# Optimization experiments

Hardware: AMD Instinct MI355X
Metric: run time of the kernel (lower is better)

## Reference

```python
import jax, jax.numpy as jnp
import numpy as np

B, N, K, H = 4, 2048, 30, 128
NODE_IN, EDGE_IN, FF = 21, 16, 4 * H


def _normalize(t, axis=-1):
    d = t / jnp.linalg.norm(t, axis=axis, keepdims=True)
    return jnp.where(jnp.isnan(d), 0.0, d)


def gather_nodes(nodes, idx):
    # nodes: [B,N,C], idx: [B,N,K] -> [B,N,K,C]
    b, n, k = idx.shape
    flat = idx.reshape(b, n * k)
    out = jnp.take_along_axis(nodes, flat[:, :, None], axis=1)
    return out.reshape(b, n, k, nodes.shape[-1])


def cal_dihedral(Xf, eps=1e-7):
    dX = Xf[:, 1:, :] - Xf[:, :-1, :]
    U = _normalize(dX)
    u0, u1, u2 = U[:, :-2], U[:, 1:-1], U[:, 2:]
    n0 = _normalize(jnp.cross(u0, u1))
    n1 = _normalize(jnp.cross(u1, u2))
    cosD = jnp.clip((n0 * n1).sum(-1), -1 + eps, 1 - eps)
    v = _normalize(jnp.cross(n0, n1))
    return jnp.sign((-v * u1).sum(-1)) * jnp.arccos(cosD)


def dihedrals(X, eps=1e-7):
    b, n = X.shape[0], X.shape[1]
    Xf = X[:, :, :3, :].reshape(b, 3 * n, 3)
    D = cal_dihedral(Xf)
    D = jnp.pad(D, ((0, 0), (1, 2))).reshape(b, n, 3)
    dihed = jnp.concatenate([jnp.cos(D), jnp.sin(D)], -1)
    dX = Xf[:, 1:] - Xf[:, :-1]
    U = _normalize(dX)
    cosA = jnp.clip((U[:, :-2] * U[:, 1:-1]).sum(-1), -1 + eps, 1 - eps)
    A = jnp.pad(jnp.arccos(cosA), ((0, 0), (1, 2))).reshape(b, n, 3)
    ang = jnp.concatenate([jnp.cos(A), jnp.sin(A)], -1)
    return jnp.concatenate([dihed, ang], -1)  # [B,N,12]


def quaternions(R):
    diag = jnp.diagonal(R, axis1=-2, axis2=-1)
    Rxx, Ryy, Rzz = diag[..., 0], diag[..., 1], diag[..., 2]
    mags = 0.5 * jnp.sqrt(jnp.abs(1 + jnp.stack([Rxx - Ryy - Rzz, -Rxx + Ryy - Rzz, -Rxx - Ryy + Rzz], -1)))
    signs = jnp.sign(jnp.stack([R[..., 2, 1] - R[..., 1, 2], R[..., 0, 2] - R[..., 2, 0], R[..., 1, 0] - R[..., 0, 1]], -1))
    xyz = signs * mags
    w = jnp.sqrt(jax.nn.relu(1 + diag.sum(-1, keepdims=True))) / 2.0
    return _normalize(jnp.concatenate([xyz, w], -1))


def orientations(X, E_idx):
    V = X  # [B,N,4,3]
    b, n = X.shape[0], X.shape[1]
    k = E_idx.shape[2]
    Xf = X[:, :, :3, :].reshape(b, 3 * n, 3)
    dX = Xf[:, 1:] - Xf[:, :-1]
    U = _normalize(dX)
    u0, u1 = U[:, :-2], U[:, 1:-1]
    n0 = _normalize(jnp.cross(u0, u1))[:, ::3]
    b1 = _normalize(u0 - u1)[:, ::3]
    Xa = Xf[:, ::3]  # [B,N,3]
    Q = jnp.stack([b1, n0, jnp.cross(b1, n0)], 2)  # [B,N-1,3,3]
    Q = Q.reshape(b, Q.shape[1], 9)
    Q = jnp.pad(Q, ((0, 0), (0, 1), (0, 0)))  # [B,N,9]
    Qn = gather_nodes(Q, E_idx).reshape(b, n, k, 3, 3)
    Xn = gather_nodes(V[:, :, 1, :], E_idx)
    Nn = gather_nodes(V[:, :, 0, :], E_idx)
    Cn = gather_nodes(V[:, :, 2, :], E_idx)
    On = gather_nodes(V[:, :, 3, :], E_idx)
    Q3 = Q.reshape(b, n, 3, 3)
    dXn = jnp.stack([Xn, Nn, Cn, On], 3) - Xa[:, :, None, None, :]  # [B,N,K,4,3]
    dU = jnp.einsum('bnij,bnkaj->bnkai', Q3, dXn)
    E_direct = _normalize(dU).reshape(b, n, k, 12)
    R = jnp.einsum('bnji,bnkjl->bnkil', Q3, Qn)  # Q^T @ Q_neighbors
    q = quaternions(R)  # [B,N,K,4]
    dX_inner = V[:, :, jnp.array([0, 2, 3]), :] - Xa[:, :, None, :]
    dU_inner = _normalize(jnp.einsum('bnij,bnaj->bnai', Q3, dX_inner))
    V_direct = dU_inner.reshape(b, n, 9)
    return V_direct, E_direct, q


def layernorm(x, g, bta, eps=1e-5):
    m = x.mean(-1, keepdims=True)
    v = ((x - m) ** 2).mean(-1, keepdims=True)
    return (x - m) / jnp.sqrt(v + eps) * g + bta


def gelu(x):
    return jax.nn.gelu(x, approximate=False)


def forward(X, E_idx, Wv_w, Wv_b, We_w, We_b, W1_w, W1_b, W2_w, W2_b, W3_w, W3_b,
            Wi_w, Wi_b, Wo_w, Wo_b, ln1_g, ln1_b, ln2_g, ln2_b):
    k = E_idx.shape[2]
    Dfeat = dihedrals(X)                     # [B,N,12]
    Vd, Ed, q = orientations(X, E_idx)       # [B,N,9],[B,N,K,12],[B,N,K,4]
    hV = jnp.concatenate([Dfeat, Vd], -1) @ Wv_w + Wv_b     # [B,N,H]
    hE = jnp.concatenate([Ed, q], -1) @ We_w + We_b         # [B,N,K,H]
    hV_nbr = gather_nodes(hV, E_idx)                        # [B,N,K,H]
    hV_exp = jnp.broadcast_to(hV[:, :, None, :], hV_nbr.shape)
    hEV = jnp.concatenate([hV_exp, hE, hV_nbr], -1)         # [B,N,K,3H]
    msg = gelu(hEV @ W1_w + W1_b)
    msg = gelu(msg @ W2_w + W2_b)
    msg = msg @ W3_w + W3_b
    dh = msg.sum(-2) / k
    hV = layernorm(hV + dh, ln1_g, ln1_b)
    ff = gelu(hV @ Wi_w + Wi_b) @ Wo_w + Wo_b
    hV = layernorm(hV + ff, ln2_g, ln2_b)
    return hV


def _lin(key, fan_in, fan_out):
    s = 1.0 / np.sqrt(fan_in)
    kw, kb = jax.random.split(key)
    return (jax.random.uniform(kw, (fan_in, fan_out), minval=-s, maxval=s),
            jax.random.uniform(kb, (fan_out,), minval=-s, maxval=s))


def setup_inputs() -> dict:
    key = jax.random.key(0)
    ks = jax.random.split(key, 10)
    X = jax.random.normal(ks[0], (B, N, 4, 3), dtype=jnp.float32) * 3.0
    E_idx = jax.random.randint(ks[1], (B, N, K), 0, N)
    Wv_w, Wv_b = _lin(ks[2], NODE_IN, H)
    We_w, We_b = _lin(ks[3], EDGE_IN, H)
    W1_w, W1_b = _lin(ks[4], 3 * H, H)
    W2_w, W2_b = _lin(ks[5], H, H)
    W3_w, W3_b = _lin(ks[6], H, H)
    Wi_w, Wi_b = _lin(ks[7], H, FF)
    Wo_w, Wo_b = _lin(ks[8], FF, H)
    return {
        'X': X, 'E_idx': E_idx,
        'Wv_w': Wv_w, 'Wv_b': Wv_b, 'We_w': We_w, 'We_b': We_b,
        'W1_w': W1_w, 'W1_b': W1_b, 'W2_w': W2_w, 'W2_b': W2_b,
        'W3_w': W3_w, 'W3_b': W3_b, 'Wi_w': Wi_w, 'Wi_b': Wi_b,
        'Wo_w': Wo_w, 'Wo_b': Wo_b,
        'ln1_g': jnp.ones((H,), jnp.float32), 'ln1_b': jnp.zeros((H,), jnp.float32),
        'ln2_g': jnp.ones((H,), jnp.float32), 'ln2_b': jnp.zeros((H,), jnp.float32),
    }


def reference(X, E_idx, Wv_w, Wv_b, We_w, We_b, W1_w, W1_b, W2_w, W2_b, W3_w, W3_b,
              Wi_w, Wi_b, Wo_w, Wo_b, ln1_g, ln1_b, ln2_g, ln2_b):
    return forward(X, E_idx, Wv_w, Wv_b, We_w, We_b, W1_w, W1_b, W2_w, W2_b,
                   W3_w, W3_b, Wi_w, Wi_b, Wo_w, Wo_b, ln1_g, ln1_b, ln2_g, ln2_b)
```

## Files before the change

kernel.cpp:

```cpp
#include <hip/hip_runtime.h>
#include <math.h>

#define BB 4
#define NN 2048
#define KNB 30
#define HH 128
#define FFD 512

typedef __attribute__((ext_vector_type(4))) float  f32x4;
typedef __attribute__((ext_vector_type(8))) short  s16x8;
typedef __attribute__((ext_vector_type(4))) short  s16x4;

struct F3 { float x,y,z; };
__device__ __forceinline__ F3 f3(float a,float b,float c){ F3 r; r.x=a; r.y=b; r.z=c; return r; }
__device__ __forceinline__ F3 sub3(F3 a, F3 b){ return f3(a.x-b.x, a.y-b.y, a.z-b.z); }
__device__ __forceinline__ float dot3(F3 a, F3 b){ return a.x*b.x + a.y*b.y + a.z*b.z; }
__device__ __forceinline__ F3 cross3(F3 a, F3 b){
  return f3(a.y*b.z-a.z*b.y, a.z*b.x-a.x*b.z, a.x*b.y-a.y*b.x);
}
__device__ __forceinline__ F3 nrm3(F3 a){
  float n2 = dot3(a,a);
  if (n2 <= 0.f) return f3(0.f,0.f,0.f);
  float inv = 1.0f/sqrtf(n2);
  return f3(a.x*inv, a.y*inv, a.z*inv);
}
__device__ __forceinline__ float sgnf(float x){ return (x>0.f)?1.f:((x<0.f)?-1.f:0.f); }
__device__ __forceinline__ float clip1(float x){
  const float e = 1e-7f;
  return fminf(fmaxf(x, -1.f+e), 1.f-e);
}
__device__ __forceinline__ float fgelu(float x){
  float x2 = x*x;
  float t = __builtin_fmaf(-0.1029641763f, x2, -2.302344055f);
  float d = 1.f + __builtin_amdgcn_exp2f(t*x);
  return x * __builtin_amdgcn_rcpf(d);
}
__device__ __forceinline__ short f2bf(float x){
  union { float f; unsigned u; } v; v.f = x;
  unsigned r = v.u + 0x7fffu + ((v.u >> 16) & 1u);
  return (short)(r >> 16);
}

__global__ void k_init(const float* __restrict__ X, float* __restrict__ Qws,
                       float* __restrict__ featws,
                       const float* __restrict__ We, const float* __restrict__ Web,
                       const float* __restrict__ W1, const float* __restrict__ W2,
                       const float* __restrict__ Wi, const float* __restrict__ Wo,
                       const float* __restrict__ W3,
                       short* __restrict__ wfoldT, float* __restrict__ bfold,
                       short* __restrict__ w2t, short* __restrict__ w1aT,
                       short* __restrict__ w1cT, short* __restrict__ wiT,
                       short* __restrict__ woT, short* __restrict__ w3T){
  if (blockIdx.x < 32){
    int t = blockIdx.x*256 + threadIdx.x;
    int b = t / NN, n = t % NN;
    const float* Xb = X + (size_t)b*NN*12;
    #define LD3(r,a) f3(Xb[((r)*4+(a))*3+0], Xb[((r)*4+(a))*3+1], Xb[((r)*4+(a))*3+2])
    F3 x0=LD3(n,0), x1=LD3(n,1), x2=LD3(n,2), x3=LD3(n,3);
    F3 U[5];
    U[1]=nrm3(sub3(x1,x0));
    U[2]=nrm3(sub3(x2,x1));
    if (n>0){ F3 p = LD3(n-1,2); U[0]=nrm3(sub3(x0,p)); } else U[0]=f3(0.f,0.f,0.f);
    if (n<NN-1){ F3 y0=LD3(n+1,0), y1=LD3(n+1,1); U[3]=nrm3(sub3(y0,x2)); U[4]=nrm3(sub3(y1,y0)); }
    else { U[3]=f3(0.f,0.f,0.f); U[4]=f3(0.f,0.f,0.f); }

    float feat[21];
    #pragma unroll
    for (int tt=0; tt<3; tt++){
      bool valid = (n>0 || tt>0) && (n<NN-1 || tt==0);
      if (valid){
        F3 a=U[tt], bv=U[tt+1], c=U[tt+2];
        F3 n0=nrm3(cross3(a,bv)), n1=nrm3(cross3(bv,c));
        float cd = clip1(dot3(n0,n1));
        F3 v = nrm3(cross3(n0,n1));
        float s = sgnf(-dot3(v,bv));
        feat[tt]   = (s==0.f) ? 1.f : cd;
        feat[3+tt] = s*sqrtf(fmaxf(1.f-cd*cd, 0.f));
        float ca = clip1(dot3(a,bv));
        feat[6+tt] = ca;
        feat[9+tt] = sqrtf(fmaxf(1.f-ca*ca, 0.f));
      } else {
        feat[tt]=1.f; feat[3+tt]=0.f; feat[6+tt]=1.f; feat[9+tt]=0.f;
      }
    }
    float Q[9];
    if (n<NN-1){
      F3 b1=nrm3(sub3(U[1],U[2]));
      F3 n0=nrm3(cross3(U[1],U[2]));
      F3 r2=cross3(b1,n0);
      Q[0]=b1.x;Q[1]=b1.y;Q[2]=b1.z;Q[3]=n0.x;Q[4]=n0.y;Q[5]=n0.z;Q[6]=r2.x;Q[7]=r2.y;Q[8]=r2.z;
    } else {
      #pragma unroll
      for (int i=0;i<9;i++) Q[i]=0.f;
    }
    float* qp = Qws + (size_t)t*9;
    #pragma unroll
    for (int i=0;i<9;i++) qp[i]=Q[i];

    feat[12]=0.f; feat[13]=0.f; feat[14]=0.f;
    F3 d1=sub3(x2,x0), d2=sub3(x3,x0);
    F3 r1 = nrm3(f3(Q[0]*d1.x+Q[1]*d1.y+Q[2]*d1.z,
                    Q[3]*d1.x+Q[4]*d1.y+Q[5]*d1.z,
                    Q[6]*d1.x+Q[7]*d1.y+Q[8]*d1.z));
    F3 r2v= nrm3(f3(Q[0]*d2.x+Q[1]*d2.y+Q[2]*d2.z,
                    Q[3]*d2.x+Q[4]*d2.y+Q[5]*d2.z,
                    Q[6]*d2.x+Q[7]*d2.y+Q[8]*d2.z));
    feat[15]=r1.x; feat[16]=r1.y; feat[17]=r1.z;
    feat[18]=r2v.x; feat[19]=r2v.y; feat[20]=r2v.z;
    float* fp = featws + (size_t)t*21;
    #pragma unroll
    for (int i=0;i<21;i++) fp[i]=feat[i];
    #undef LD3
    return;
  }
  int t = (blockIdx.x-32)*256 + threadIdx.x;
  if (t < 2048){
    int c = t >> 4, j = t & 15;
    float a = 0.f;
    for (int k=0;k<HH;k++) a += We[j*HH+k]*W1[(HH+k)*HH + c];
    wfoldT[t] = f2bf(a);
  } else if (t < 2176){
    int c = t - 2048;
    float a = 0.f;
    for (int k=0;k<HH;k++) a += Web[k]*W1[(HH+k)*HH + c];
    bfold[c] = a;
  } else if (t < 18560){
    int i = t - 2176;  int n = i >> 7, k = i & 127;
    w2t[n*HH + k] = f2bf(W2[k*HH + n]);
  } else if (t < 34944){
    int i = t - 18560; int n = i >> 7, k = i & 127;
    w1aT[n*HH + k] = f2bf(W1[k*HH + n]);
  } else if (t < 51328){
    int i = t - 34944; int n = i >> 7, k = i & 127;
    w1cT[n*HH + k] = f2bf(W1[(256+k)*HH + n]);
  } else if (t < 116864){
    int i = t - 51328; int n = i >> 7, k = i & 127;
    wiT[n*HH + k] = f2bf(Wi[k*FFD + n]);
  } else if (t < 182400){
    int i = t - 116864; int k = i >> 7, n = i & 127;
    woT[n*FFD + k] = f2bf(Wo[k*HH + n]);
  } else if (t < 198784){
    int i = t - 182400; int n = i >> 7, k = i & 127;
    w3T[n*HH + k] = f2bf(W3[k*HH + n]);
  }
}

#define ENB 8
#define PNB 32
__global__ void k_ep(const float* __restrict__ X, const int* __restrict__ Eidx,
                     const float* __restrict__ Qws, short* __restrict__ efB,
                     const float* __restrict__ featws, const float* __restrict__ Wv,
                     const float* __restrict__ Wvb, const short* __restrict__ w1aT,
                     const short* __restrict__ w1cT, const float* __restrict__ W1b,
                     const float* __restrict__ bfold, float* __restrict__ hVws,
                     float* __restrict__ Sws, float* __restrict__ Gws){
  const int tid = threadIdx.x;
  if (blockIdx.x < BB*NN/ENB){
    const int nn = tid >> 5, slot = tid & 31;
    const int gnode = blockIdx.x*ENB + nn;
    const int b = gnode >> 11;
    const int n = gnode & (NN-1);
    const int bofs = b*NN;
    short out[16];
    if (slot < KNB){
      int j = Eidx[(size_t)gnode*KNB + slot];
      const float* Qs = Qws + (size_t)gnode*9;
      float q[9];
      #pragma unroll
      for (int i=0;i<9;i++) q[i]=Qs[i];
      const float* Xb = X + (size_t)b*NN*12;
      F3 Xa = f3(Xb[n*12+0], Xb[n*12+1], Xb[n*12+2]);
      const float* Xn = Xb + (size_t)j*12;
      F3 A[4];
      A[0] = f3(Xn[3],  Xn[4],  Xn[5]);
      A[1] = f3(Xn[0],  Xn[1],  Xn[2]);
      A[2] = f3(Xn[6],  Xn[7],  Xn[8]);
      A[3] = f3(Xn[9],  Xn[10], Xn[11]);
      #pragma unroll
      for (int a=0;a<4;a++){
        F3 d = sub3(A[a], Xa);
        F3 w = f3(q[0]*d.x+q[1]*d.y+q[2]*d.z,
                  q[3]*d.x+q[4]*d.y+q[5]*d.z,
                  q[6]*d.x+q[7]*d.y+q[8]*d.z);
        F3 wn = nrm3(w);
        out[a*3+0] = f2bf(wn.x);
        out[a*3+1] = f2bf(wn.y);
        out[a*3+2] = f2bf(wn.z);
      }
      const float* Qn = Qws + (size_t)(bofs + j)*9;
      float p[9];
      #pragma unroll
      for (int i=0;i<9;i++) p[i]=Qn[i];
      float R00=q[0]*p[0]+q[3]*p[3]+q[6]*p[6];
      float R01=q[0]*p[1]+q[3]*p[4]+q[6]*p[7];
      float R02=q[0]*p[2]+q[3]*p[5]+q[6]*p[8];
      float R10=q[1]*p[0]+q[4]*p[3]+q[7]*p[6];
      float R11=q[1]*p[1]+q[4]*p[4]+q[7]*p[7];
      float R12=q[1]*p[2]+q[4]*p[5]+q[7]*p[8];
      float R20=q[2]*p[0]+q[5]*p[3]+q[8]*p[6];
      float R21=q[2]*p[1]+q[5]*p[4]+q[8]*p[7];
      float R22=q[2]*p[2]+q[5]*p[5]+q[8]*p[8];
      float mx = 0.5f*sqrtf(fabsf(1.f+R00-R11-R22));
      float my = 0.5f*sqrtf(fabsf(1.f-R00+R11-R22));
      float mz = 0.5f*sqrtf(fabsf(1.f-R00-R11+R22));
      float qx = sgnf(R21-R12)*mx;
      float qy = sgnf(R02-R20)*my;
      float qz = sgnf(R10-R01)*mz;
      float qw = 0.5f*sqrtf(fmaxf(1.f+R00+R11+R22, 0.f));
      float n2 = qx*qx+qy*qy+qz*qz+qw*qw;
      float inv = (n2>0.f) ? 1.f/sqrtf(n2) : 0.f;
      out[12]=f2bf(qx*inv); out[13]=f2bf(qy*inv);
      out[14]=f2bf(qz*inv); out[15]=f2bf(qw*inv);
    } else {
      #pragma unroll
      for (int i=0;i<16;i++) out[i]=0;
    }
    short* dst = efB + ((size_t)gnode*32 + slot)*16;
    *reinterpret_cast<s16x8*>(dst)   = *reinterpret_cast<s16x8*>(&out[0]);
    *reinterpret_cast<s16x8*>(dst+8) = *reinterpret_cast<s16x8*>(&out[8]);
    return;
  }
  __shared__ __align__(16) short hvL[PNB][136];
  int base = (blockIdx.x - BB*NN/ENB)*PNB;
  {
    int c = tid & 127, half = tid >> 7;
    float wv[21];
    #pragma unroll
    for (int j=0;j<21;j++) wv[j] = Wv[j*HH + c];
    float wb = Wvb[c];
    #pragma unroll 2
    for (int it=0; it<16; ++it){
      int g = it*2 + half;
      const float* f = featws + (size_t)(base+g)*21;
      float a = wb;
      #pragma unroll
      for (int j=0;j<21;j++) a += f[j]*wv[j];
      hVws[(size_t)(base+g)*HH + c] = a;
      hvL[g][c] = f2bf(a);
    }
  }
  __syncthreads();
  {
    int l = tid & 63, w = tid >> 6;
    int lr = l & 15, lg = l >> 4;
    int m = w & 1;
    int nbase = (w >> 1)*4;
    s16x8 afr[4];
    #pragma unroll
    for (int ks=0; ks<4; ks++)
      afr[ks] = *reinterpret_cast<const s16x8*>(&hvL[m*16 + lr][ks*32 + lg*8]);
    f32x4 Cs[4], Cg[4];
    #pragma unroll
    for (int q=0;q<4;q++){ Cs[q]=(f32x4){0,0,0,0}; Cg[q]=(f32x4){0,0,0,0}; }
    #pragma unroll
    for (int q=0;q<4;q++){
      int ncol = (nbase+q)*16 + lr;
      #pragma unroll
      for (int ks=0; ks<4; ks++){
        s16x8 ba = *reinterpret_cast<const s16x8*>(&w1aT[ncol*HH + ks*32 + lg*8]);
        s16x8 bc = *reinterpret_cast<const s16x8*>(&w1cT[ncol*HH + ks*32 + lg*8]);
        Cs[q] = __builtin_amdgcn_mfma_f32_16x16x32_bf16(afr[ks], ba, Cs[q], 0,0,0);
        Cg[q] = __builtin_amdgcn_mfma_f32_16x16x32_bf16(afr[ks], bc, Cg[q], 0,0,0);
      }
    }
    #pragma unroll
    for (int q=0;q<4;q++){
      int ncol = (nbase+q)*16 + lr;
      float bc = W1b[ncol] + bfold[ncol];
      #pragma unroll
      for (int i=0;i<4;i++){
        int row = m*16 + lg*4 + i;
        size_t o = (size_t)(base+row)*HH + ncol;
        Sws[o] = Cs[q][i] + bc;
        Gws[o] = Cg[q][i];
      }
    }
  }
}

#define NPB 4
#define A2STR 136
__launch_bounds__(256, 4)
__global__ void k_msg(const int* __restrict__ Eidx, const short* __restrict__ efB,
                      const float* __restrict__ Sws, const float* __restrict__ Gws,
                      const short* __restrict__ wfoldT, const short* __restrict__ w2t,
                      const float* __restrict__ W2b, float* __restrict__ csws){
  __shared__ __align__(16) short A2s[128*A2STR];

  const int tid = threadIdx.x;
  const int gbase = blockIdx.x*NPB;
  const int b = gbase >> 11;
  const int bofs = b*NN;

  const int w  = tid >> 6;
  const int l  = tid & 63;
  const int lr = l & 15;
  const int lg = l >> 4;
  const int gnode = gbase + w;

  const bool ok1 = (lr < KNB - 16);
  int j0 = Eidx[(size_t)gnode*KNB + lr];
  int j1 = ok1 ? Eidx[(size_t)gnode*KNB + 16 + lr] : 0;

  {
    const float* g0 = Gws + (size_t)(bofs + j0)*HH;
    const float* g1 = Gws + (size_t)(bofs + j1)*HH;
    const float* Srow = Sws + (size_t)gnode*HH;
    s16x8 wf[8];
    #pragma unroll
    for (int ct=0; ct<8; ct++){
      if (lg < 2)
        wf[ct] = *reinterpret_cast<const s16x8*>(&wfoldT[(ct*16+lr)*16 + lg*8]);
      else
        wf[ct] = (s16x8){0,0,0,0,0,0,0,0};
    }
    const short* efn = efB + (size_t)gnode*32*16;
    s16x8 ef[2];
    #pragma unroll
    for (int rt=0; rt<2; rt++){
      if (lg < 2)
        ef[rt] = *reinterpret_cast<const s16x8*>(&efn[(rt*16 + lr)*16 + lg*8]);
      else
        ef[rt] = (s16x8){0,0,0,0,0,0,0,0};
    }
    const int e0 = w*32 + lr;
    const int e1 = e0 + 16;
    #pragma unroll
    for (int ct=0; ct<8; ct++){
      const int cbase = ct*16 + lg*4;
      f32x4 S4 = *reinterpret_cast<const f32x4*>(Srow + cbase);
      f32x4 G0 = *reinterpret_cast<const f32x4*>(g0 + cbase);
      f32x4 G1 = *reinterpret_cast<const f32x4*>(g1 + cbase);
      f32x4 C0 = __builtin_amdgcn_mfma_f32_16x16x32_bf16(wf[ct], ef[0], (f32x4){0,0,0,0}, 0,0,0);
      f32x4 C1 = __builtin_amdgcn_mfma_f32_16x16x32_bf16(wf[ct], ef[1], (f32x4){0,0,0,0}, 0,0,0);
      s16x4 o0, o1;
      #pragma unroll
      for (int i=0;i<4;i++){
        o0[i] = f2bf(fgelu(C0[i] + S4[i] + G0[i]));
        float v1 = fgelu(C1[i] + S4[i] + G1[i]);
        o1[i] = ok1 ? f2bf(v1) : (short)0;
      }
      *reinterpret_cast<s16x4*>(&A2s[e0*A2STR + cbase]) = o0;
      *reinterpret_cast<s16x4*>(&A2s[e1*A2STR + cbase]) = o1;
    }
  }

  {
    f32x4 Cacc[2][8];
    #pragma unroll
    for (int mt=0; mt<2; mt++)
      #pragma unroll
      for (int nt=0; nt<8; nt++)
        Cacc[mt][nt] = (f32x4){0.f,0.f,0.f,0.f};
    #pragma unroll
    for (int ks=0; ks<4; ks++){
      const int koff = ks*32 + lg*8;
      s16x8 a0 = *reinterpret_cast<const s16x8*>(&A2s[(w*32      + lr)*A2STR + koff]);
      s16x8 a1 = *reinterpret_cast<const s16x8*>(&A2s[(w*32 + 16 + lr)*A2STR + koff]);
      #pragma unroll
      for (int nt=0; nt<8; nt++){
        s16x8 bv = *reinterpret_cast<const s16x8*>(&w2t[(lr + nt*16)*HH + koff]);
        Cacc[0][nt] = __builtin_amdgcn_mfma_f32_16x16x32_bf16(a0, bv, Cacc[0][nt], 0,0,0);
        Cacc[1][nt] = __builtin_amdgcn_mfma_f32_16x16x32_bf16(a1, bv, Cacc[1][nt], 0,0,0);
      }
    }
    float* csrow = csws + (size_t)gnode*HH;
    #pragma unroll
    for (int nt=0; nt<8; nt++){
      float b2v = W2b[lr + nt*16];
      float part = 0.f;
      #pragma unroll
      for (int mt=0; mt<2; mt++){
        #pragma unroll
        for (int i=0; i<4; i++){
          int row32 = mt*16 + lg*4 + i;
          float v = fgelu(Cacc[mt][nt][i] + b2v);
          if (row32 < KNB) part += v;
        }
      }
      part += __shfl_xor(part, 16, 64);
      part += __shfl_xor(part, 32, 64);
      if (l < 16) csrow[nt*16 + lr] = part;
    }
  }
}

#define FNB 16
__global__ void k_ffn(const float* __restrict__ csws, const float* __restrict__ hVws,
                      const short* __restrict__ w3T, const float* __restrict__ W3b,
                      const short* __restrict__ wiT, const short* __restrict__ woT,
                      const float* __restrict__ Wib, const float* __restrict__ Wob,
                      const float* __restrict__ l1g, const float* __restrict__ l1b,
                      const float* __restrict__ l2g, const float* __restrict__ l2b,
                      float* __restrict__ out){
  __shared__ __align__(16) short hv1[FNB][136];
  __shared__ __align__(16) float yL[FNB][HH];
  __shared__ __align__(16) short ffh[FNB][520];
  __shared__ float partS[FNB][4], partQ[FNB][4];
  const int tid = threadIdx.x;
  const int l = tid & 63, w = tid >> 6;
  const int base = blockIdx.x*FNB;
  const int lr = l & 15, lg = l >> 4;

  {
    int i0 = tid*8;
    int row = i0 >> 7, col = i0 & 127;
    const float* p = csws + (size_t)(base+row)*HH + col;
    f32x4 a = *reinterpret_cast<const f32x4*>(p);
    f32x4 bq = *reinterpret_cast<const f32x4*>(p+4);
    s16x8 v;
    #pragma unroll
    for (int j=0;j<4;j++){ v[j]=f2bf(a[j]); v[4+j]=f2bf(bq[j]); }
    *reinterpret_cast<s16x8*>(&hv1[row][col]) = v;
  }
  __syncthreads();

  {
    s16x8 acs[4];
    #pragma unroll
    for (int ks=0; ks<4; ks++)
      acs[ks] = *reinterpret_cast<const s16x8*>(&hv1[lr][ks*32 + lg*8]);
    f32x4 Cd[2];
    Cd[0]=(f32x4){0,0,0,0}; Cd[1]=(f32x4){0,0,0,0};
    #pragma unroll
    for (int t2=0; t2<2; t2++){
      int ncol = (2*w+t2)*16 + lr;
      #pragma unroll
      for (int ks=0; ks<4; ks++){
        s16x8 bv = *reinterpret_cast<const s16x8*>(&w3T[ncol*HH + ks*32 + lg*8]);
        Cd[t2] = __builtin_amdgcn_mfma_f32_16x16x32_bf16(acs[ks], bv, Cd[t2], 0,0,0);
      }
    }
    float vv[2][4];
    float ps[4] = {0,0,0,0}, pq[4] = {0,0,0,0};
    #pragma unroll
    for (int t2=0; t2<2; t2++){
      int col = (2*w+t2)*16 + lr;
      float b3 = W3b[col];
      #pragma unroll
      for (int i=0;i<4;i++){
        int row = lg*4 + i;
        float v = hVws[(size_t)(base+row)*HH + col] + Cd[t2][i]*(1.f/30.f) + b3;
        vv[t2][i] = v;
        ps[i] += v; pq[i] += v*v;
      }
    }
    #pragma unroll
    for (int i=0;i<4;i++){
      #pragma unroll
      for (int o=1;o<16;o<<=1){
        ps[i] += __shfl_xor(ps[i], o, 64);
        pq[i] += __shfl_xor(pq[i], o, 64);
      }
      if (lr == 0){ partS[lg*4+i][w] = ps[i]; partQ[lg*4+i][w] = pq[i]; }
    }
    __syncthreads();
    #pragma unroll
    for (int t2=0; t2<2; t2++){
      int col = (2*w+t2)*16 + lr;
      float g1 = l1g[col], b1 = l1b[col];
      #pragma unroll
      for (int i=0;i<4;i++){
        int row = lg*4 + i;
        float S = partS[row][0]+partS[row][1]+partS[row][2]+partS[row][3];
        float Q = partQ[row][0]+partQ[row][1]+partQ[row][2]+partQ[row][3];
        float m = S*(1.f/HH);
        float inv = 1.f/sqrtf(Q*(1.f/HH) - m*m + 1e-5f);
        float y = (vv[t2][i]-m)*inv*g1 + b1;
        yL[row][col] = y;
        hv1[row][col] = f2bf(y);
      }
    }
  }
  __syncthreads();

  {
    s16x8 afr[4];
    #pragma unroll
    for (int ks=0; ks<4; ks++)
      afr[ks] = *reinterpret_cast<const s16x8*>(&hv1[lr][ks*32 + lg*8]);
    #pragma unroll
    for (int q=0; q<8; q++){
      int ncol = (w*8+q)*16 + lr;
      f32x4 C = (f32x4){0,0,0,0};
      #pragma unroll
      for (int ks=0; ks<4; ks++){
        s16x8 bv = *reinterpret_cast<const s16x8*>(&wiT[ncol*HH + ks*32 + lg*8]);
        C = __builtin_amdgcn_mfma_f32_16x16x32_bf16(afr[ks], bv, C, 0,0,0);
      }
      float bi = Wib[ncol];
      #pragma unroll
      for (int i=0;i<4;i++){
        int row = lg*4 + i;
        ffh[row][ncol] = f2bf(fgelu(C[i] + bi));
      }
    }
  }
  __syncthreads();

  f32x4 C2[2];
  C2[0]=(f32x4){0,0,0,0}; C2[1]=(f32x4){0,0,0,0};
  for (int ks=0; ks<16; ++ks){
    s16x8 a = *reinterpret_cast<const s16x8*>(&ffh[lr][ks*32 + lg*8]);
    #pragma unroll
    for (int t2=0; t2<2; t2++){
      int ncol = (2*w+t2)*16 + lr;
      s16x8 bv = *reinterpret_cast<const s16x8*>(&woT[ncol*FFD + ks*32 + lg*8]);
      C2[t2] = __builtin_amdgcn_mfma_f32_16x16x32_bf16(a, bv, C2[t2], 0,0,0);
    }
  }
  float vv[2][4];
  float ps[4] = {0,0,0,0}, pq[4] = {0,0,0,0};
  #pragma unroll
  for (int t2=0; t2<2; t2++){
    int col = (2*w+t2)*16 + lr;
    float bo = Wob[col];
    #pragma unroll
    for (int i=0;i<4;i++){
      int row = lg*4 + i;
      float v = yL[row][col] + C2[t2][i] + bo;
      vv[t2][i] = v;
      ps[i] += v; pq[i] += v*v;
    }
  }
  #pragma unroll
  for (int i=0;i<4;i++){
    #pragma unroll
    for (int o=1;o<16;o<<=1){
      ps[i] += __shfl_xor(ps[i], o, 64);
      pq[i] += __shfl_xor(pq[i], o, 64);
    }
    if (lr == 0){ partS[lg*4+i][w] = ps[i]; partQ[lg*4+i][w] = pq[i]; }
  }
  __syncthreads();
  float mean[4], inv[4];
  #pragma unroll
  for (int i=0;i<4;i++){
    int row = lg*4 + i;
    float S = partS[row][0]+partS[row][1]+partS[row][2]+partS[row][3];
    float Q = partQ[row][0]+partQ[row][1]+partQ[row][2]+partQ[row][3];
    float m = S*(1.f/HH);
    float var = Q*(1.f/HH) - m*m;
    mean[i] = m;
    inv[i] = 1.f/sqrtf(var + 1e-5f);
  }
  #pragma unroll
  for (int t2=0; t2<2; t2++){
    int col = (2*w+t2)*16 + lr;
    float g2 = l2g[col], b2 = l2b[col];
    #pragma unroll
    for (int i=0;i<4;i++){
      int row = lg*4 + i;
      out[(size_t)(base+row)*HH + col] = (vv[t2][i]-mean[i])*inv[i]*g2 + b2;
    }
  }
}

extern "C" void kernel_launch(void* const* d_in, const int* in_sizes, int n_in,
                              void* d_out, int out_size, void* d_ws, size_t ws_size,
                              hipStream_t stream) {
  (void)in_sizes; (void)n_in; (void)out_size; (void)ws_size;
  const float* X   = (const float*)d_in[0];
  const int*   Ei  = (const int*)  d_in[1];
  const float* Wv  = (const float*)d_in[2];
  const float* Wvb = (const float*)d_in[3];
  const float* We  = (const float*)d_in[4];
  const float* Web = (const float*)d_in[5];
  const float* W1  = (const float*)d_in[6];
  const float* W1b = (const float*)d_in[7];
  const float* W2  = (const float*)d_in[8];
  const float* W2b = (const float*)d_in[9];
  const float* W3  = (const float*)d_in[10];
  const float* W3b = (const float*)d_in[11];
  const float* Wi  = (const float*)d_in[12];
  const float* Wib = (const float*)d_in[13];
  const float* Wo  = (const float*)d_in[14];
  const float* Wob = (const float*)d_in[15];
  const float* l1g = (const float*)d_in[16];
  const float* l1b = (const float*)d_in[17];
  const float* l2g = (const float*)d_in[18];
  const float* l2b = (const float*)d_in[19];
  float* out = (float*)d_out;

  float* wsf    = (float*)d_ws;
  float* featws = wsf + 0;
  float* Qws    = wsf + 172032;
  float* hVws   = wsf + 245760;
  float* Gws    = wsf + 1294336;
  float* Sws    = wsf + 2342912;
  float* csws   = wsf + 3391488;
  short* efB    = (short*)(wsf + 4440064);
  short* wfoldT = (short*)(wsf + 6537216);
  float* bfold  = wsf + 6538240;
  short* w2t    = (short*)(wsf + 6538368);
  short* w1aT   = (short*)(wsf + 6546560);
  short* w1cT   = (short*)(wsf + 6554752);
  short* wiT    = (short*)(wsf + 6562944);
  short* woT    = (short*)(wsf + 6595712);
  short* w3T    = (short*)(wsf + 6628480);

  k_init<<<dim3(809), dim3(256), 0, stream>>>(X, Qws, featws, We, Web, W1, W2, Wi, Wo, W3,
                                              wfoldT, bfold, w2t, w1aT, w1cT, wiT, woT, w3T);
  k_ep  <<<dim3(BB*NN/ENB + BB*NN/PNB), dim3(256), 0, stream>>>(
            X, Ei, Qws, efB, featws, Wv, Wvb, w1aT, w1cT, W1b, bfold, hVws, Sws, Gws);
  k_msg <<<dim3(BB*NN/NPB), dim3(256), 0, stream>>>(Ei, efB, Sws, Gws,
                                                    wfoldT, w2t, W2b, csws);
  k_ffn <<<dim3(BB*NN/FNB), dim3(256), 0, stream>>>(csws, hVws, w3T, W3b, wiT, woT,
                                                    Wib, Wob, l1g, l1b, l2g, l2b, out);
}
```

Baseline: 200.0 us.

## Fuse message kernel and FFN kernel into one kernel with shared-memory handoff

Merges the per-node message aggregation kernel and the node FFN/LayerNorm kernel into one kernel. Each block loops over 16 nodes in 4 groups, keeps the aggregated messages in LDS, and reuses the message buffer's LDS for the FFN staging arrays. This removes a global write/read of the aggregate tensor and one kernel launch. The cost is fewer blocks (a quarter as many), extra barriers per group, and lower occupancy from the changed launch bounds.

```diff
diff --git a/kernel.cpp b/kernel.cpp
--- a/kernel.cpp
+++ b/kernel.cpp
@@ -278,140 +278,134 @@
   }
 }
 
-#define NPB 4
+#define FNB 16
 #define A2STR 136
-__launch_bounds__(256, 4)
-__global__ void k_msg(const int* __restrict__ Eidx, const short* __restrict__ efB,
-                      const float* __restrict__ Sws, const float* __restrict__ Gws,
-                      const short* __restrict__ wfoldT, const short* __restrict__ w2t,
-                      const float* __restrict__ W2b, float* __restrict__ csws){
+__launch_bounds__(256, 2)
+__global__ void k_fused(const int* __restrict__ Eidx, const short* __restrict__ efB,
+                        const float* __restrict__ Sws, const float* __restrict__ Gws,
+                        const short* __restrict__ wfoldT, const short* __restrict__ w2t,
+                        const float* __restrict__ W2b,
+                        const float* __restrict__ hVws,
+                        const short* __restrict__ w3T, const float* __restrict__ W3b,
+                        const short* __restrict__ wiT, const short* __restrict__ woT,
+                        const float* __restrict__ Wib, const float* __restrict__ Wob,
+                        const float* __restrict__ l1g, const float* __restrict__ l1b,
+                        const float* __restrict__ l2g, const float* __restrict__ l2b,
+                        float* __restrict__ out){
   __shared__ __align__(16) short A2s[128*A2STR];
+  __shared__ __align__(16) float csL[FNB][HH];
+  __shared__ float partS[FNB][4], partQ[FNB][4];
+  short* hv1b = A2s;
+  float* yLb  = (float*)(A2s + 2176);
+  short* ffhb = A2s + 6272;
 
   const int tid = threadIdx.x;
-  const int gbase = blockIdx.x*NPB;
-  const int b = gbase >> 11;
+  const int base = blockIdx.x*FNB;
+  const int b = base >> 11;
   const int bofs = b*NN;
-
   const int w  = tid >> 6;
   const int l  = tid & 63;
   const int lr = l & 15;
   const int lg = l >> 4;
-  const int gnode = gbase + w;
-
+
+  s16x8 wf[8];
+  #pragma unroll
+  for (int ct=0; ct<8; ct++){
+    if (lg < 2)
+      wf[ct] = *reinterpret_cast<const s16x8*>(&wfoldT[(ct*16+lr)*16 + lg*8]);
+    else
+      wf[ct] = (s16x8){0,0,0,0,0,0,0,0};
+  }
   const bool ok1 = (lr < KNB - 16);
-  int j0 = Eidx[(size_t)gnode*KNB + lr];
-  int j1 = ok1 ? Eidx[(size_t)gnode*KNB + 16 + lr] : 0;
-
-  {
-    const float* g0 = Gws + (size_t)(bofs + j0)*HH;
-    const float* g1 = Gws + (size_t)(bofs + j1)*HH;
-    const float* Srow = Sws + (size_t)gnode*HH;
-    s16x8 wf[8];
-    #pragma unroll
-    for (int ct=0; ct<8; ct++){
-      if (lg < 2)
-        wf[ct] = *reinterpret_cast<const s16x8*>(&wfoldT[(ct*16+lr)*16 + lg*8]);
-      else
-        wf[ct] = (s16x8){0,0,0,0,0,0,0,0};
-    }
-    const short* efn = efB + (size_t)gnode*32*16;
-    s16x8 ef[2];
-    #pragma unroll
-    for (int rt=0; rt<2; rt++){
-      if (lg < 2)
-        ef[rt] = *reinterpret_cast<const s16x8*>(&efn[(rt*16 + lr)*16 + lg*8]);
-      else
-        ef[rt] = (s16x8){0,0,0,0,0,0,0,0};
-    }
-    const int e0 = w*32 + lr;
-    const int e1 = e0 + 16;
-    #pragma unroll
-    for (int ct=0; ct<8; ct++){
-      const int cbase = ct*16 + lg*4;
-      f32x4 S4 = *reinterpret_cast<const f32x4*>(Srow + cbase);
-      f32x4 G0 = *reinterpret_cast<const f32x4*>(g0 + cbase);
-      f32x4 G1 = *reinterpret_cast<const f32x4*>(g1 + cbase);
-      f32x4 C0 = __builtin_amdgcn_mfma_f32_16x16x32_bf16(wf[ct], ef[0], (f32x4){0,0,0,0}, 0,0,0);
-      f32x4 C1 = __builtin_amdgcn_mfma_f32_16x16x32_bf16(wf[ct], ef[1], (f32x4){0,0,0,0}, 0,0,0);
-      s16x4 o0, o1;
-      #pragma unroll
-      for (int i=0;i<4;i++){
-        o0[i] = f2bf(fgelu(C0[i] + S4[i] + G0[i]));
-        float v1 = fgelu(C1[i] + S4[i] + G1[i]);
-        o1[i] = ok1 ? f2bf(v1) : (short)0;
-      }
-      *reinterpret_cast<s16x4*>(&A2s[e0*A2STR + cbase]) = o0;
-      *reinterpret_cast<s16x4*>(&A2s[e1*A2STR + cbase]) = o1;
-    }
-  }
-
-  {
-    f32x4 Cacc[2][8];
-    #pragma unroll
-    for (int mt=0; mt<2; mt++)
-      #pragma unroll
-      for (int nt=0; nt<8; nt++)
-        Cacc[mt][nt] = (f32x4){0.f,0.f,0.f,0.f};
-    #pragma unroll
-    for (int ks=0; ks<4; ks++){
-      const int koff = ks*32 + lg*8;
-      s16x8 a0 = *reinterpret_cast<const s16x8*>(&A2s[(w*32      + lr)*A2STR + koff]);
-      s16x8 a1 = *reinterpret_cast<const s16x8*>(&A2s[(w*32 + 16 + lr)*A2STR + koff]);
+
+  for (int g=0; g<4; ++g){
+    const int ln = g*4 + w;
+    const int gnode = base + ln;
+    {
+      int j0 = Eidx[(size_t)gnode*KNB + lr];
+      int j1 = ok1 ? Eidx[(size_t)gnode*KNB + 16 + lr] : 0;
+      const float* g0 = Gws + (size_t)(bofs + j0)*HH;
+      const float* g1 = Gws + (size_t)(bofs + j1)*HH;
+      const float* Srow = Sws + (size_t)gnode*HH;
+      const short* efn = efB + (size_t)gnode*32*16;
+      s16x8 ef[2];
+      #pragma unroll
+      for (int rt=0; rt<2; rt++){
+        if (lg < 2)
+          ef[rt] = *reinterpret_cast<const s16x8*>(&efn[(rt*16 + lr)*16 + lg*8]);
+        else
+          ef[rt] = (s16x8){0,0,0,0,0,0,0,0};
+      }
+      const int e0 = w*32 + lr;
+      const int e1 = e0 + 16;
+      #pragma unroll
+      for (int ct=0; ct<8; ct++){
+        const int cbase = ct*16 + lg*4;
+        f32x4 S4 = *reinterpret_cast<const f32x4*>(Srow + cbase);
+        f32x4 G0 = *reinterpret_cast<const f32x4*>(g0 + cbase);
+        f32x4 G1 = *reinterpret_cast<const f32x4*>(g1 + cbase);
+        f32x4 C0 = __builtin_amdgcn_mfma_f32_16x16x32_bf16(wf[ct], ef[0], (f32x4){0,0,0,0}, 0,0,0);
+        f32x4 C1 = __builtin_amdgcn_mfma_f32_16x16x32_bf16(wf[ct], ef[1], (f32x4){0,0,0,0}, 0,0,0);
+        s16x4 o0, o1;
+        #pragma unroll
+        for (int i=0;i<4;i++){
+          o0[i] = f2bf(fgelu(C0[i] + S4[i] + G0[i]));
+          float v1 = fgelu(C1[i] + S4[i] + G1[i]);
+          o1[i] = ok1 ? f2bf(v1) : (short)0;
+        }
+        *reinterpret_cast<s16x4*>(&A2s[e0*A2STR + cbase]) = o0;
+        *reinterpret_cast<s16x4*>(&A2s[e1*A2STR + cbase]) = o1;
+      }
+    }
+    __syncthreads();
+    {
+      f32x4 Cacc[2][8];
+      #pragma unroll
+      for (int mt=0; mt<2; mt++)
+        #pragma unroll
+        for (int nt=0; nt<8; nt++)
+          Cacc[mt][nt] = (f32x4){0.f,0.f,0.f,0.f};
+      #pragma unroll
+      for (int ks=0; ks<4; ks++){
+        const int koff = ks*32 + lg*8;
+        s16x8 a0 = *reinterpret_cast<const s16x8*>(&A2s[(w*32      + lr)*A2STR + koff]);
+        s16x8 a1 = *reinterpret_cast<const s16x8*>(&A2s[(w*32 + 16 + lr)*A2STR + koff]);
+        #pragma unroll
+        for (int nt=0; nt<8; nt++){
+          s16x8 bv = *reinterpret_cast<const s16x8*>(&w2t[(lr + nt*16)*HH + koff]);
+          Cacc[0][nt] = __builtin_amdgcn_mfma_f32_16x16x32_bf16(a0, bv, Cacc[0][nt], 0,0,0);
+          Cacc[1][nt] = __builtin_amdgcn_mfma_f32_16x16x32_bf16(a1, bv, Cacc[1][nt], 0,0,0);
+        }
+      }
       #pragma unroll
       for (int nt=0; nt<8; nt++){
-        s16x8 bv = *reinterpret_cast<const s16x8*>(&w2t[(lr + nt*16)*HH + koff]);
-        Cacc[0][nt] = __builtin_amdgcn_mfma_f32_16x16x32_bf16(a0, bv, Cacc[0][nt], 0,0,0);
-        Cacc[1][nt] = __builtin_amdgcn_mfma_f32_16x16x32_bf16(a1, bv, Cacc[1][nt], 0,0,0);
-      }
-    }
-    float* csrow = csws + (size_t)gnode*HH;
-    #pragma unroll
-    for (int nt=0; nt<8; nt++){
-      float b2v = W2b[lr + nt*16];
-      float part = 0.f;
-      #pragma unroll
-      for (int mt=0; mt<2; mt++){
+        float b2v = W2b[lr + nt*16];
+        float part = 0.f;
         #pragma unroll
-        for (int i=0; i<4; i++){
-          int row32 = mt*16 + lg*4 + i;
-          float v = fgelu(Cacc[mt][nt][i] + b2v);
-          if (row32 < KNB) part += v;
+        for (int mt=0; mt<2; mt++){
+          #pragma unroll
+          for (int i=0; i<4; i++){
+            int row32 = mt*16 + lg*4 + i;
+            float v = fgelu(Cacc[mt][nt][i] + b2v);
+            if (row32 < KNB) part += v;
+          }
         }
-      }
-      part += __shfl_xor(part, 16, 64);
-      part += __shfl_xor(part, 32, 64);
-      if (l < 16) csrow[nt*16 + lr] = part;
-    }
-  }
-}
-
-#define FNB 16
-__global__ void k_ffn(const float* __restrict__ csws, const float* __restrict__ hVws,
-                      const short* __restrict__ w3T, const float* __restrict__ W3b,
-                      const short* __restrict__ wiT, const short* __restrict__ woT,
-                      const float* __restrict__ Wib, const float* __restrict__ Wob,
-                      const float* __restrict__ l1g, const float* __restrict__ l1b,
-                      const float* __restrict__ l2g, const float* __restrict__ l2b,
-                      float* __restrict__ out){
-  __shared__ __align__(16) short hv1[FNB][136];
-  __shared__ __align__(16) float yL[FNB][HH];
-  __shared__ __align__(16) short ffh[FNB][520];
-  __shared__ float partS[FNB][4], partQ[FNB][4];
-  const int tid = threadIdx.x;
-  const int l = tid & 63, w = tid >> 6;
-  const int base = blockIdx.x*FNB;
-  const int lr = l & 15, lg = l >> 4;
+        part += __shfl_xor(part, 16, 64);
+        part += __shfl_xor(part, 32, 64);
+        if (l < 16) csL[ln][nt*16 + lr] = part;
+      }
+    }
+    __syncthreads();
+  }
 
   {
     int i0 = tid*8;
     int row = i0 >> 7, col = i0 & 127;
-    const float* p = csws + (size_t)(base+row)*HH + col;
-    f32x4 a = *reinterpret_cast<const f32x4*>(p);
-    f32x4 bq = *reinterpret_cast<const f32x4*>(p+4);
+    const float* p = &csL[row][col];
     s16x8 v;
     #pragma unroll
-    for (int j=0;j<4;j++){ v[j]=f2bf(a[j]); v[4+j]=f2bf(bq[j]); }
-    *reinterpret_cast<s16x8*>(&hv1[row][col]) = v;
+    for (int j=0;j<8;j++) v[j] = f2bf(p[j]);
+    *reinterpret_cast<s16x8*>(&hv1b[row*136 + col]) = v;
   }
   __syncthreads();
 
@@ -419,7 +413,7 @@
     s16x8 acs[4];
     #pragma unroll
     for (int ks=0; ks<4; ks++)
-      acs[ks] = *reinterpret_cast<const s16x8*>(&hv1[lr][ks*32 + lg*8]);
+      acs[ks] = *reinterpret_cast<const s16x8*>(&hv1b[lr*136 + ks*32 + lg*8]);
     f32x4 Cd[2];
     Cd[0]=(f32x4){0,0,0,0}; Cd[1]=(f32x4){0,0,0,0};
     #pragma unroll
@@ -467,8 +461,8 @@
         float m = S*(1.f/HH);
         float inv = 1.f/sqrtf(Q*(1.f/HH) - m*m + 1e-5f);
         float y = (vv[t2][i]-m)*inv*g1 + b1;
-        yL[row][col] = y;
-        hv1[row][col] = f2bf(y);
+        yLb[row*HH + col] = y;
+        hv1b[row*136 + col] = f2bf(y);
       }
     }
   }
@@ -478,7 +472,7 @@
     s16x8 afr[4];
     #pragma unroll
     for (int ks=0; ks<4; ks++)
-      afr[ks] = *reinterpret_cast<const s16x8*>(&hv1[lr][ks*32 + lg*8]);
+      afr[ks] = *reinterpret_cast<const s16x8*>(&hv1b[lr*136 + ks*32 + lg*8]);
     #pragma unroll
     for (int q=0; q<8; q++){
       int ncol = (w*8+q)*16 + lr;
@@ -492,7 +486,7 @@
       #pragma unroll
       for (int i=0;i<4;i++){
         int row = lg*4 + i;
-        ffh[row][ncol] = f2bf(fgelu(C[i] + bi));
+        ffhb[row*520 + ncol] = f2bf(fgelu(C[i] + bi));
       }
     }
   }
@@ -501,7 +495,7 @@
   f32x4 C2[2];
   C2[0]=(f32x4){0,0,0,0}; C2[1]=(f32x4){0,0,0,0};
   for (int ks=0; ks<16; ++ks){
-    s16x8 a = *reinterpret_cast<const s16x8*>(&ffh[lr][ks*32 + lg*8]);
+    s16x8 a = *reinterpret_cast<const s16x8*>(&ffhb[lr*520 + ks*32 + lg*8]);
     #pragma unroll
     for (int t2=0; t2<2; t2++){
       int ncol = (2*w+t2)*16 + lr;
@@ -518,7 +512,7 @@
     #pragma unroll
     for (int i=0;i<4;i++){
       int row = lg*4 + i;
-      float v = yL[row][col] + C2[t2][i] + bo;
+      float v = yLb[row*HH + col] + C2[t2][i] + bo;
       vv[t2][i] = v;
       ps[i] += v; pq[i] += v*v;
     }
@@ -588,23 +582,21 @@
   float* hVws   = wsf + 245760;
   float* Gws    = wsf + 1294336;
   float* Sws    = wsf + 2342912;
-  float* csws   = wsf + 3391488;
-  short* efB    = (short*)(wsf + 4440064);
-  short* wfoldT = (short*)(wsf + 6537216);
-  float* bfold  = wsf + 6538240;
-  short* w2t    = (short*)(wsf + 6538368);
-  short* w1aT   = (short*)(wsf + 6546560);
-  short* w1cT   = (short*)(wsf + 6554752);
-  short* wiT    = (short*)(wsf + 6562944);
-  short* woT    = (short*)(wsf + 6595712);
-  short* w3T    = (short*)(wsf + 6628480);
-
-  k_init<<<dim3(809), dim3(256), 0, stream>>>(X, Qws, featws, We, Web, W1, W2, Wi, Wo, W3,
-                                              wfoldT, bfold, w2t, w1aT, w1cT, wiT, woT, w3T);
-  k_ep  <<<dim3(BB*NN/ENB + BB*NN/PNB), dim3(256), 0, stream>>>(
-            X, Ei, Qws, efB, featws, Wv, Wvb, w1aT, w1cT, W1b, bfold, hVws, Sws, Gws);
-  k_msg <<<dim3(BB*NN/NPB), dim3(256), 0, stream>>>(Ei, efB, Sws, Gws,
-                                                    wfoldT, w2t, W2b, csws);
-  k_ffn <<<dim3(BB*NN/FNB), dim3(256), 0, stream>>>(csws, hVws, w3T, W3b, wiT, woT,
-                                                    Wib, Wob, l1g, l1b, l2g, l2b, out);
-}
+  short* efB    = (short*)(wsf + 3391488);
+  short* wfoldT = (short*)(wsf + 5488640);
+  float* bfold  = wsf + 5489664;
+  short* w2t    = (short*)(wsf + 5489792);
+  short* w1aT   = (short*)(wsf + 5497984);
+  short* w1cT   = (short*)(wsf + 5506176);
+  short* wiT    = (short*)(wsf + 5514368);
+  short* woT    = (short*)(wsf + 5547136);
+  short* w3T    = (short*)(wsf + 5579904);
+
+  k_init <<<dim3(809), dim3(256), 0, stream>>>(X, Qws, featws, We, Web, W1, W2, Wi, Wo, W3,
+                                               wfoldT, bfold, w2t, w1aT, w1cT, wiT, woT, w3T);
+  k_ep   <<<dim3(BB*NN/ENB + BB*NN/PNB), dim3(256), 0, stream>>>(
+             X, Ei, Qws, efB, featws, Wv, Wvb, w1aT, w1cT, W1b, bfold, hVws, Sws, Gws);
+  k_fused<<<dim3(BB*NN/FNB), dim3(256), 0, stream>>>(
+             Ei, efB, Sws, Gws, wfoldT, w2t, W2b, hVws, w3T, W3b, wiT, woT,
+             Wib, Wob, l1g, l1b, l2g, l2b, out);
+}
```

Measured after the change: 188.1 us. -6.0%, faster.
